# Kernel optimization log

Measured on AMD Instinct MI355X. Metric: run time of the kernel, lower is better.

Reference implementation:

```python
import jax, jax.numpy as jnp
import numpy as np

NEG_SLOPE = 0.2  # PyG GATConv default leaky_relu slope


def gat_conv(x, src, dst, W, att_src, att_dst, bias, num_nodes):
    """PyG-style GATConv with concat=False (mean over heads).
    x: [N, Fin], src/dst: [E] (self-loops already appended),
    W: [Fin, H*C], att_src/att_dst: [H, C], bias: [C].
    """
    H, C = att_src.shape
    h = (x @ W).reshape(num_nodes, H, C)               # [N, H, C]
    a_s = jnp.sum(h * att_src[None], axis=-1)          # [N, H]
    a_d = jnp.sum(h * att_dst[None], axis=-1)          # [N, H]
    e = jax.nn.leaky_relu(a_s[src] + a_d[dst], NEG_SLOPE)  # [E, H]
    # softmax over incoming edges per destination node
    e_max = jax.ops.segment_max(e, dst, num_segments=num_nodes)  # [N, H]
    e_exp = jnp.exp(e - e_max[dst])
    denom = jax.ops.segment_sum(e_exp, dst, num_segments=num_nodes)
    alpha = e_exp / (denom[dst] + 1e-16)               # [E, H]
    msg = h[src] * alpha[:, :, None]                   # [E, H, C]
    out = jax.ops.segment_sum(msg, dst, num_segments=num_nodes)  # [N, H, C]
    return out.mean(axis=1) + bias                     # concat=False -> head mean


def setup_inputs() -> dict:
    N, E = 100000, 1600000
    Fin, Hid, Fout, Hds = 128, 64, 32, 2
    key = jax.random.key(0)
    ks = jax.random.split(key, 12)
    glorot = lambda k, shape, fan: (jax.random.normal(k, shape, jnp.float32) / np.sqrt(fan))
    return {
        "x": jax.random.normal(ks[0], (N, Fin), jnp.float32),
        "edge_index": jax.random.randint(ks[1], (2, E), 0, N, jnp.int64 if jax.config.read("jax_enable_x64") else jnp.int32),
        "W1": glorot(ks[2], (Fin, Hds * Hid), Fin),
        "att_src1": glorot(ks[3], (Hds, Hid), Hid),
        "att_dst1": glorot(ks[4], (Hds, Hid), Hid),
        "b1": jnp.zeros((Hid,), jnp.float32),
        "W2": glorot(ks[5], (Hid, Hds * Fout), Hid),
        "att_src2": glorot(ks[6], (Hds, Fout), Fout),
        "att_dst2": glorot(ks[7], (Hds, Fout), Fout),
        "b2": jnp.zeros((Fout,), jnp.float32),
    }


def reference(x, edge_index, W1, att_src1, att_dst1, b1, W2, att_src2, att_dst2, b2):
    N = x.shape[0]
    # PyG GATConv default: add self-loops
    loops = jnp.arange(N, dtype=edge_index.dtype)
    src = jnp.concatenate([edge_index[0], loops])
    dst = jnp.concatenate([edge_index[1], loops])
    # dropout(p=0.6) is identity in eval mode
    h = gat_conv(x, src, dst, W1, att_src1, att_dst1, b1, N)
    h = jax.nn.elu(h)
    out = gat_conv(h, src, dst, W2, att_src2, att_dst2, b2, N)
    return out
```

## Files before the change

### kernel.cpp

```cpp
#include <hip/hip_runtime.h>
#include <hip/hip_bf16.h>
#include <hip/hip_fp16.h>
#include <math.h>


#define BINBITS 9
#define NBUCK 256
#define CHUNK 4096
#define SPANCAP 12288


__global__ void init_kernel(int* __restrict__ bcnt) {
    bcnt[threadIdx.x] = 0;
}

__global__ void bucket_hist_kernel(const int* __restrict__ dst, int* __restrict__ bcnt, int E) {
    __shared__ int h[NBUCK];
    int t = threadIdx.x;
    h[t] = 0;
    __syncthreads();
    for (int i = blockIdx.x * blockDim.x + t; i < E; i += gridDim.x * blockDim.x)
        atomicAdd(&h[dst[i] >> BINBITS], 1);
    __syncthreads();
    if (h[t]) atomicAdd(&bcnt[t], h[t]);
}

__global__ void bucket_scan_kernel(const int* __restrict__ bcnt, int* __restrict__ bbase,
                                   int* __restrict__ bfill) {
    __shared__ int sd[NBUCK];
    int t = threadIdx.x;
    int v = bcnt[t];
    sd[t] = v;
    __syncthreads();
    for (int o = 1; o < NBUCK; o <<= 1) {
        int x = (t >= o) ? sd[t - o] : 0;
        __syncthreads();
        sd[t] += x;
        __syncthreads();
    }
    int exc = sd[t] - v;
    bbase[t] = exc;
    bfill[t] = exc;
    if (t == NBUCK - 1) bbase[NBUCK] = sd[t];
}

__launch_bounds__(256)
__global__ void binA_kernel(const int* __restrict__ esrc, const int* __restrict__ edst,
                            int* __restrict__ bfill, unsigned* __restrict__ binned, int E) {
    __shared__ unsigned stage[CHUNK];
    __shared__ int hcnt[NBUCK], hexc[NBUCK], gb[NBUCK], hfill[NBUCK];
    const int tid = threadIdx.x;
    const int c0 = blockIdx.x * CHUNK;
    const int n = min(CHUNK, E - c0);

    hcnt[tid] = 0;
    hfill[tid] = 0;
    __syncthreads();
    for (int i = tid; i < n; i += 256) atomicAdd(&hcnt[edst[c0 + i] >> BINBITS], 1);
    __syncthreads();
    int myc = hcnt[tid];
    hexc[tid] = myc;
    __syncthreads();
    for (int o = 1; o < NBUCK; o <<= 1) {
        int x = (tid >= o) ? hexc[tid - o] : 0;
        __syncthreads();
        hexc[tid] += x;
        __syncthreads();
    }
    hexc[tid] -= myc;
    gb[tid] = myc ? atomicAdd(&bfill[tid], myc) : 0;
    __syncthreads();

    for (int i = tid; i < n; i += 256) {
        int d = edst[c0 + i], s = esrc[c0 + i];
        int b = d >> BINBITS;
        int p = hexc[b] + atomicAdd(&hfill[b], 1);
        stage[p] = ((unsigned)(d & ((1 << BINBITS) - 1)) << 17) | (unsigned)s;
    }
    __syncthreads();

    const int wid = tid >> 6, lane = tid & 63;
    for (int b = wid * 64; b < wid * 64 + 64; ++b) {
        int cnt = hcnt[b], sb = hexc[b], g = gb[b];
        for (int l = lane; l < cnt; l += 64) binned[g + l] = stage[sb + l];
    }
}

__launch_bounds__(256)
__global__ void binB_kernel(const unsigned* __restrict__ binned, const int* __restrict__ bbase,
                            int* __restrict__ rowptr, int* __restrict__ csr, int N) {
    __shared__ int cnt[512];
    __shared__ int chunk[256];
    __shared__ int excl[513];
    __shared__ int stag[SPANCAP];
    const int tid = threadIdx.x;
    const int b = blockIdx.x;
    const int node0 = b << BINBITS;
    if (node0 >= N) return;
    const int nn = min(512, N - node0);

    cnt[tid] = (tid < nn) ? 1 : 0;
    cnt[tid + 256] = (tid + 256 < nn) ? 1 : 0;
    __syncthreads();
    const int e0 = bbase[b], e1 = bbase[b + 1];
    for (int i = e0 + tid; i < e1; i += 256)
        atomicAdd(&cnt[binned[i] >> 17], 1);
    __syncthreads();

    int c0v = cnt[2 * tid], c1v = cnt[2 * tid + 1];
    chunk[tid] = c0v + c1v;
    __syncthreads();
    int v = chunk[tid];
    for (int o = 1; o < 256; o <<= 1) {
        int x = (tid >= o) ? chunk[tid - o] : 0;
        __syncthreads();
        chunk[tid] += x;
        __syncthreads();
    }
    int cpre = chunk[tid] - v;
    excl[2 * tid] = cpre;
    excl[2 * tid + 1] = cpre + c0v;
    if (tid == 255) excl[512] = cpre + c0v + c1v;
    __syncthreads();

    const int rbase = e0 + node0;
    for (int i = tid; i < nn; i += 256) rowptr[node0 + i] = rbase + excl[i];
    if (node0 + nn >= N && tid == 0) rowptr[N] = rbase + excl[512];

    cnt[tid] = 0;
    cnt[tid + 256] = 0;
    __syncthreads();
    const int span = excl[512];

    if (span <= SPANCAP) {
        for (int i = e0 + tid; i < e1; i += 256) {
            unsigned e = binned[i];
            int dloc = e >> 17, src = e & 0x1FFFF;
            int p = excl[dloc] + atomicAdd(&cnt[dloc], 1);
            stag[p] = src;
        }
        for (int i = tid; i < nn; i += 256) {
            int p = excl[i] + atomicAdd(&cnt[i], 1);
            stag[p] = node0 + i;
        }
        __syncthreads();
        for (int i = tid; i < span; i += 256) csr[rbase + i] = stag[i];
    } else {
        for (int i = e0 + tid; i < e1; i += 256) {
            unsigned e = binned[i];
            int dloc = e >> 17, src = e & 0x1FFFF;
            csr[rbase + excl[dloc] + atomicAdd(&cnt[dloc], 1)] = src;
        }
        for (int i = tid; i < nn; i += 256)
            csr[rbase + excl[i] + atomicAdd(&cnt[i], 1)] = node0 + i;
    }
}


template <int FIN, int FOUT, int TM, int KC>
__launch_bounds__(256)
__global__ void gemm_attn_kernel(const float* __restrict__ X, const float* __restrict__ Wg,
                                 const float* __restrict__ atts, const float* __restrict__ attd,
                                 __half* __restrict__ Hh, float* __restrict__ a_s,
                                 float* __restrict__ a_d, int N) {
    constexpr int COLG = FOUT / 8;
    constexpr int ROWG = 256 / COLG;
    constexpr int BM = ROWG * TM;
    constexpr int C = FOUT / 2;
    constexpr int PR = BM + 4;
    __shared__ float sW[KC * FOUT];
    __shared__ float sX[KC * PR];

    const int tid = threadIdx.x;
    const int tc = tid % COLG;
    const int tr = tid / COLG;
    const int row0 = blockIdx.x * BM;

    float accA[TM][4], accB[TM][4];
#pragma unroll
    for (int i = 0; i < TM; ++i)
#pragma unroll
        for (int j = 0; j < 4; ++j) { accA[i][j] = 0.f; accB[i][j] = 0.f; }

    for (int kc = 0; kc < FIN; kc += KC) {
        __syncthreads();
        for (int idx = tid; idx < KC * FOUT / 4; idx += 256) {
            int k = idx / (FOUT / 4), cq = idx % (FOUT / 4);
            *(float4*)&sW[k * FOUT + cq * 4] =
                *(const float4*)&Wg[(size_t)(kc + k) * FOUT + cq * 4];
        }
        for (int idx = tid; idx < BM * KC / 4; idx += 256) {
            int r = idx / (KC / 4), kq = idx % (KC / 4);
            int gr = row0 + r;
            float4 v = make_float4(0.f, 0.f, 0.f, 0.f);
            if (gr < N) v = *(const float4*)&X[(size_t)gr * FIN + kc + kq * 4];
            sX[(kq * 4 + 0) * PR + r] = v.x;
            sX[(kq * 4 + 1) * PR + r] = v.y;
            sX[(kq * 4 + 2) * PR + r] = v.z;
            sX[(kq * 4 + 3) * PR + r] = v.w;
        }
        __syncthreads();
#pragma unroll 4
        for (int k = 0; k < KC; ++k) {
            float xv[TM];
#pragma unroll
            for (int q = 0; q < TM / 4; ++q)
                *(float4*)&xv[q * 4] = *(const float4*)&sX[k * PR + tr * TM + q * 4];
            float wa[4], wb[4];
            *(float4*)wa = *(const float4*)&sW[k * FOUT + tc * 4];
            *(float4*)wb = *(const float4*)&sW[k * FOUT + C + tc * 4];
#pragma unroll
            for (int i = 0; i < TM; ++i) {
#pragma unroll
                for (int j = 0; j < 4; ++j) {
                    accA[i][j] = fmaf(xv[i], wa[j], accA[i][j]);
                    accB[i][j] = fmaf(xv[i], wb[j], accB[i][j]);
                }
            }
        }
    }

    float aSA[4], aSB[4], aDA[4], aDB[4];
#pragma unroll
    for (int j = 0; j < 4; ++j) {
        aSA[j] = atts[tc * 4 + j];
        aSB[j] = atts[C + tc * 4 + j];
        aDA[j] = attd[tc * 4 + j];
        aDB[j] = attd[C + tc * 4 + j];
    }

#pragma unroll
    for (int i = 0; i < TM; ++i) {
        int gr = row0 + tr * TM + i;
        if (gr < N) {
            union { int2 i2; __half2 h2[2]; } u;
            u.h2[0] = __halves2half2(__float2half(accA[i][0]), __float2half(accA[i][1]));
            u.h2[1] = __halves2half2(__float2half(accA[i][2]), __float2half(accA[i][3]));
            *reinterpret_cast<int2*>(&Hh[(size_t)gr * FOUT + tc * 4]) = u.i2;
            u.h2[0] = __halves2half2(__float2half(accB[i][0]), __float2half(accB[i][1]));
            u.h2[1] = __halves2half2(__float2half(accB[i][2]), __float2half(accB[i][3]));
            *reinterpret_cast<int2*>(&Hh[(size_t)gr * FOUT + C + tc * 4]) = u.i2;
        }
        float ps0 = 0.f, ps1 = 0.f, pd0 = 0.f, pd1 = 0.f;
#pragma unroll
        for (int j = 0; j < 4; ++j) {
            ps0 = fmaf(accA[i][j], aSA[j], ps0);
            ps1 = fmaf(accB[i][j], aSB[j], ps1);
            pd0 = fmaf(accA[i][j], aDA[j], pd0);
            pd1 = fmaf(accB[i][j], aDB[j], pd1);
        }
#pragma unroll
        for (int o = 1; o < COLG; o <<= 1) {
            ps0 += __shfl_xor(ps0, o);
            ps1 += __shfl_xor(ps1, o);
            pd0 += __shfl_xor(pd0, o);
            pd1 += __shfl_xor(pd1, o);
        }
        if (tc == 0 && gr < N) {
            *(float2*)&a_s[gr * 2] = make_float2(ps0, ps1);
            *(float2*)&a_d[gr * 2] = make_float2(pd0, pd1);
        }
    }
}


__device__ __forceinline__ float lrelu02(float x) { return x > 0.f ? x : 0.2f * x; }

__launch_bounds__(256)
__global__ void edge_w_kernel(const float* __restrict__ a_s, const float* __restrict__ a_d,
                              const int* __restrict__ rowptr, const int* __restrict__ csr,
                              float2* __restrict__ w, int N) {
    const int wid = threadIdx.x >> 6, lane = threadIdx.x & 63;
    int n = blockIdx.x * 4 + wid;
    if (n >= N) return;
    int start = rowptr[n], end = rowptr[n + 1];
    float2 adn = ((const float2*)a_d)[n];
    float d0 = 0.f, d1 = 0.f;
    for (int j = start + lane; j < end; j += 64) {
        int s = csr[j];
        float2 asv = ((const float2*)a_s)[s];
        float e0 = __expf(lrelu02(asv.x + adn.x));
        float e1 = __expf(lrelu02(asv.y + adn.y));
        d0 += e0;
        d1 += e1;
        w[j] = make_float2(e0, e1);
    }
#pragma unroll
    for (int o = 32; o > 0; o >>= 1) {
        d0 += __shfl_xor(d0, o);
        d1 += __shfl_xor(d1, o);
    }
    float i0 = 0.5f / d0, i1 = 0.5f / d1;
    for (int j = start + lane; j < end; j += 64) {
        float2 f = w[j];
        w[j] = make_float2(f.x * i0, f.y * i1);
    }
}


template <int C, bool ELU>
__launch_bounds__(256)
__global__ void aggregate_kernel(const __half* __restrict__ Hh, const float2* __restrict__ w,
                                 const int* __restrict__ rowptr, const int* __restrict__ csr,
                                 const float* __restrict__ bias, float* __restrict__ out, int N) {
    __shared__ float2 swH[4][64][2];
    const int wid = threadIdx.x >> 6;
    const int lane = threadIdx.x & 63;
    const int hp = lane >> 5;
    const int sub = lane & 31;
    const int head = sub >> 4;
    const int chq = sub & 15;
    int n = blockIdx.x * 4 + wid;
    if (n >= N) return;
    int start = rowptr[n], end = rowptr[n + 1];

    float acc0 = 0.f, acc1 = 0.f, acc2 = 0.f, acc3 = 0.f;

    for (int cs = start; cs < end; cs += 64) {
        int j = cs + lane;
        float2 wv = make_float2(0.f, 0.f);
        int s = 0;
        if (j < end) {
            s = csr[j];
            wv = w[j];
        }
        float fs = __int_as_float(s);
        swH[wid][lane][0] = make_float2(wv.x, fs);
        swH[wid][lane][1] = make_float2(wv.y, fs);
        int cnt = min(64, end - cs);
        int npair = (cnt + 1) >> 1;
        for (int p0 = 0; p0 < npair; p0 += 4) {
            float2 e[4];
#pragma unroll
            for (int u = 0; u < 4; ++u)
                e[u] = swH[wid][2 * (p0 + u) + hp][head];
            if (C == 64) {
                ushort4 hv[4];
#pragma unroll
                for (int u = 0; u < 4; ++u)
                    hv[u] = ((const ushort4*)Hh)[(size_t)__float_as_int(e[u].y) * 32 + sub];
#pragma unroll
                for (int u = 0; u < 4; ++u) {
                    const __half* hx = (const __half*)&hv[u];
                    acc0 = fmaf(e[u].x, __half2float(hx[0]), acc0);
                    acc1 = fmaf(e[u].x, __half2float(hx[1]), acc1);
                    acc2 = fmaf(e[u].x, __half2float(hx[2]), acc2);
                    acc3 = fmaf(e[u].x, __half2float(hx[3]), acc3);
                }
            } else {
                __half2 hv[4];
#pragma unroll
                for (int u = 0; u < 4; ++u)
                    hv[u] = ((const __half2*)Hh)[(size_t)__float_as_int(e[u].y) * 32 + sub];
#pragma unroll
                for (int u = 0; u < 4; ++u) {
                    float2 v = __half22float2(hv[u]);
                    acc0 = fmaf(e[u].x, v.x, acc0);
                    acc1 = fmaf(e[u].x, v.y, acc1);
                }
            }
        }
    }

    acc0 += __shfl_xor(acc0, 32);
    acc1 += __shfl_xor(acc1, 32);
    if (C == 64) {
        acc2 += __shfl_xor(acc2, 32);
        acc3 += __shfl_xor(acc3, 32);
    }
    acc0 += __shfl_xor(acc0, 16);
    acc1 += __shfl_xor(acc1, 16);
    if (C == 64) {
        acc2 += __shfl_xor(acc2, 16);
        acc3 += __shfl_xor(acc3, 16);
    }

    if (lane < 16) {
        if (C == 64) {
            float4 bv = *(const float4*)(bias + chq * 4);
            float o0 = acc0 + bv.x;
            float o1 = acc1 + bv.y;
            float o2 = acc2 + bv.z;
            float o3 = acc3 + bv.w;
            if (ELU) {
                o0 = o0 > 0.f ? o0 : expm1f(o0);
                o1 = o1 > 0.f ? o1 : expm1f(o1);
                o2 = o2 > 0.f ? o2 : expm1f(o2);
                o3 = o3 > 0.f ? o3 : expm1f(o3);
            }
            *(float4*)(out + (size_t)n * 64 + chq * 4) = make_float4(o0, o1, o2, o3);
        } else {
            float2 bv = *(const float2*)(bias + chq * 2);
            float o0 = acc0 + bv.x;
            float o1 = acc1 + bv.y;
            if (ELU) {
                o0 = o0 > 0.f ? o0 : expm1f(o0);
                o1 = o1 > 0.f ? o1 : expm1f(o1);
            }
            *(float2*)(out + (size_t)n * 32 + chq * 2) = make_float2(o0, o1);
        }
    }
}


extern "C" void kernel_launch(void* const* d_in, const int* in_sizes, int n_in,
                              void* d_out, int out_size, void* d_ws, size_t ws_size,
                              hipStream_t stream) {
    const float* x    = (const float*)d_in[0];
    const int*   eidx = (const int*)d_in[1];
    const float* W1   = (const float*)d_in[2];
    const float* as1w = (const float*)d_in[3];
    const float* ad1w = (const float*)d_in[4];
    const float* b1   = (const float*)d_in[5];
    const float* W2   = (const float*)d_in[6];
    const float* as2w = (const float*)d_in[7];
    const float* ad2w = (const float*)d_in[8];
    const float* b2   = (const float*)d_in[9];
    float* out = (float*)d_out;

    const int N = in_sizes[0] / 128;
    const int E = in_sizes[1] / 2;
    const int NBK = (N + (1 << BINBITS) - 1) >> BINBITS;

    char* base = (char*)d_ws;
    size_t off = 0;
    auto alloc = [&](size_t bytes) {
        size_t cur = off;
        off += (bytes + 255) & ~(size_t)255;
        return (void*)(base + cur);
    };

    int* rowptr   = (int*)alloc((size_t)(N + 1) * 4);
    int* csr      = (int*)alloc((size_t)(E + N) * 4);
    int* bcnt     = (int*)alloc((size_t)NBUCK * 4);
    int* bbase    = (int*)alloc((size_t)(NBUCK + 1) * 4);
    int* bfill    = (int*)alloc((size_t)NBUCK * 4);
    unsigned* binned = (unsigned*)alloc((size_t)E * 4);
    __half* h1    = (__half*)alloc((size_t)N * 128 * 2);
    float* x2     = (float*)alloc((size_t)N * 64 * 4);
    float* a_s    = (float*)alloc((size_t)N * 2 * 4);
    float* a_d    = (float*)alloc((size_t)N * 2 * 4);
    float2* wEdge = (float2*)alloc((size_t)(E + N) * 8);

    const int* esrc = eidx;
    const int* edst = eidx + E;

    init_kernel<<<1, NBUCK, 0, stream>>>(bcnt);
    bucket_hist_kernel<<<256, 256, 0, stream>>>(edst, bcnt, E);
    bucket_scan_kernel<<<1, NBUCK, 0, stream>>>(bcnt, bbase, bfill);
    binA_kernel<<<(E + CHUNK - 1) / CHUNK, 256, 0, stream>>>(esrc, edst, bfill, binned, E);
    binB_kernel<<<NBK, 256, 0, stream>>>(binned, bbase, rowptr, csr, N);

    gemm_attn_kernel<128, 128, 8, 32>
        <<<(N + 127) / 128, 256, 0, stream>>>(x, W1, as1w, ad1w, h1, a_s, a_d, N);
    edge_w_kernel<<<(N + 3) / 4, 256, 0, stream>>>(a_s, a_d, rowptr, csr, wEdge, N);
    aggregate_kernel<64, true><<<(N + 3) / 4, 256, 0, stream>>>(h1, wEdge, rowptr, csr, b1, x2, N);

    gemm_attn_kernel<64, 64, 4, 32>
        <<<(N + 127) / 128, 256, 0, stream>>>(x2, W2, as2w, ad2w, h1, a_s, a_d, N);
    edge_w_kernel<<<(N + 3) / 4, 256, 0, stream>>>(a_s, a_d, rowptr, csr, wEdge, N);
    aggregate_kernel<32, false><<<(N + 3) / 4, 256, 0, stream>>>(h1, wEdge, rowptr, csr, b2, out, N);
}
```

Before: 396.9 us.

## Use fp16 MFMA for node projection GEMMs and store hidden features in fp16

Replaces the scalar fp32 FMA GEMM with a matrix-core kernel using 16x16x32 fp16 MFMA, with weights pre-transposed and converted to fp16 by a small kernel. The first layer's aggregation now writes its ELU output in fp16, which the second GEMM reads directly, halving that intermediate's traffic. Attention logits are computed from the MFMA accumulators, and the H tile is staged through shared memory for coalesced stores. Inputs are rounded to fp16 before the multiply, which lowers precision. The whole A tile sits in shared memory (about 64 KB for layer 1), which may limit occupancy.

```diff
diff --git a/kernel.cpp b/kernel.cpp
--- a/kernel.cpp
+++ b/kernel.cpp
@@ -8,6 +8,9 @@
 #define NBUCK 256
 #define CHUNK 4096
 #define SPANCAP 12288
+
+typedef _Float16 half8 __attribute__((ext_vector_type(8)));
+typedef float f32x4 __attribute__((ext_vector_type(4)));
 
 
 __global__ void init_kernel(int* __restrict__ bcnt) {
@@ -157,109 +160,139 @@
 }
 
 
-template <int FIN, int FOUT, int TM, int KC>
+__global__ void wcvt_kernel(const float* __restrict__ W, _Float16* __restrict__ Wt,
+                            int K, int Fout) {
+    int i = blockIdx.x * 256 + threadIdx.x;
+    if (i < K * Fout) {
+        int n = i / K, k = i % K;
+        Wt[i] = (_Float16)W[k * Fout + n];
+    }
+}
+
+
+template <int FIN, int FOUT, typename XT>
 __launch_bounds__(256)
-__global__ void gemm_attn_kernel(const float* __restrict__ X, const float* __restrict__ Wg,
-                                 const float* __restrict__ atts, const float* __restrict__ attd,
-                                 __half* __restrict__ Hh, float* __restrict__ a_s,
-                                 float* __restrict__ a_d, int N) {
-    constexpr int COLG = FOUT / 8;
-    constexpr int ROWG = 256 / COLG;
-    constexpr int BM = ROWG * TM;
+__global__ void gemm_attn_mfma(const XT* __restrict__ X, const _Float16* __restrict__ Wt,
+                               const float* __restrict__ atts, const float* __restrict__ attd,
+                               __half* __restrict__ Hh, float* __restrict__ a_s,
+                               float* __restrict__ a_d, int N) {
+    constexpr int BM = 128;
     constexpr int C = FOUT / 2;
-    constexpr int PR = BM + 4;
-    __shared__ float sW[KC * FOUT];
-    __shared__ float sX[KC * PR];
+    constexpr int NT = FOUT / 16;
+    constexpr int KS = FIN / 32;
+    constexpr int HT = C / 16;
+    __shared__ _Float16 sA[BM * FIN];
+    __shared__ _Float16 sB[FOUT * FIN];
 
     const int tid = threadIdx.x;
-    const int tc = tid % COLG;
-    const int tr = tid / COLG;
+    const int wv = tid >> 6, ln = tid & 63;
+    const int lm = ln & 15, quad = ln >> 4;
     const int row0 = blockIdx.x * BM;
 
-    float accA[TM][4], accB[TM][4];
-#pragma unroll
-    for (int i = 0; i < TM; ++i)
-#pragma unroll
-        for (int j = 0; j < 4; ++j) { accA[i][j] = 0.f; accB[i][j] = 0.f; }
-
-    for (int kc = 0; kc < FIN; kc += KC) {
-        __syncthreads();
-        for (int idx = tid; idx < KC * FOUT / 4; idx += 256) {
-            int k = idx / (FOUT / 4), cq = idx % (FOUT / 4);
-            *(float4*)&sW[k * FOUT + cq * 4] =
-                *(const float4*)&Wg[(size_t)(kc + k) * FOUT + cq * 4];
-        }
-        for (int idx = tid; idx < BM * KC / 4; idx += 256) {
-            int r = idx / (KC / 4), kq = idx % (KC / 4);
+    if (sizeof(XT) == 4) {
+        for (int idx = tid; idx < BM * FIN / 4; idx += 256) {
+            int r = idx / (FIN / 4), c4 = idx % (FIN / 4);
             int gr = row0 + r;
             float4 v = make_float4(0.f, 0.f, 0.f, 0.f);
-            if (gr < N) v = *(const float4*)&X[(size_t)gr * FIN + kc + kq * 4];
-            sX[(kq * 4 + 0) * PR + r] = v.x;
-            sX[(kq * 4 + 1) * PR + r] = v.y;
-            sX[(kq * 4 + 2) * PR + r] = v.z;
-            sX[(kq * 4 + 3) * PR + r] = v.w;
-        }
-        __syncthreads();
-#pragma unroll 4
-        for (int k = 0; k < KC; ++k) {
-            float xv[TM];
-#pragma unroll
-            for (int q = 0; q < TM / 4; ++q)
-                *(float4*)&xv[q * 4] = *(const float4*)&sX[k * PR + tr * TM + q * 4];
-            float wa[4], wb[4];
-            *(float4*)wa = *(const float4*)&sW[k * FOUT + tc * 4];
-            *(float4*)wb = *(const float4*)&sW[k * FOUT + C + tc * 4];
-#pragma unroll
-            for (int i = 0; i < TM; ++i) {
-#pragma unroll
-                for (int j = 0; j < 4; ++j) {
-                    accA[i][j] = fmaf(xv[i], wa[j], accA[i][j]);
-                    accB[i][j] = fmaf(xv[i], wb[j], accB[i][j]);
+            if (gr < N) v = *(const float4*)&((const float*)X)[(size_t)gr * FIN + c4 * 4];
+            _Float16 h4[4] = {(_Float16)v.x, (_Float16)v.y, (_Float16)v.z, (_Float16)v.w};
+            *(float2*)&sA[r * FIN + c4 * 4] = *(float2*)h4;
+        }
+    } else {
+        for (int idx = tid; idx < BM * FIN / 8; idx += 256) {
+            int r = idx / (FIN / 8), c8 = idx % (FIN / 8);
+            int gr = row0 + r;
+            int4 v = make_int4(0, 0, 0, 0);
+            if (gr < N) v = *(const int4*)&((const __half*)X)[(size_t)gr * FIN + c8 * 8];
+            *(int4*)&sA[r * FIN + c8 * 8] = v;
+        }
+    }
+    for (int idx = tid; idx < FOUT * FIN / 8; idx += 256)
+        *(int4*)&sB[idx * 8] = *(const int4*)&Wt[idx * 8];
+    __syncthreads();
+
+    f32x4 acc[2][NT];
+#pragma unroll
+    for (int mt = 0; mt < 2; ++mt)
+#pragma unroll
+        for (int nt = 0; nt < NT; ++nt) acc[mt][nt] = f32x4{0.f, 0.f, 0.f, 0.f};
+
+    const int r0 = wv * 32 + lm;
+#pragma unroll
+    for (int ks = 0; ks < KS; ++ks) {
+        int k0 = ks * 32 + quad * 8;
+        half8 a0 = *(const half8*)&sA[r0 * FIN + k0];
+        half8 a1 = *(const half8*)&sA[(r0 + 16) * FIN + k0];
+#pragma unroll
+        for (int nt = 0; nt < NT; ++nt) {
+            half8 b = *(const half8*)&sB[(nt * 16 + lm) * FIN + k0];
+            acc[0][nt] = __builtin_amdgcn_mfma_f32_16x16x32_f16(a0, b, acc[0][nt], 0, 0, 0);
+            acc[1][nt] = __builtin_amdgcn_mfma_f32_16x16x32_f16(a1, b, acc[1][nt], 0, 0, 0);
+        }
+    }
+
+    float psum[2][4][2], pdum[2][4][2];
+#pragma unroll
+    for (int mt = 0; mt < 2; ++mt)
+#pragma unroll
+        for (int r = 0; r < 4; ++r) {
+            psum[mt][r][0] = psum[mt][r][1] = 0.f;
+            pdum[mt][r][0] = pdum[mt][r][1] = 0.f;
+        }
+#pragma unroll
+    for (int nt = 0; nt < NT; ++nt) {
+        float av = atts[nt * 16 + lm];
+        float dv = attd[nt * 16 + lm];
+        int hh = nt / HT;
+#pragma unroll
+        for (int mt = 0; mt < 2; ++mt)
+#pragma unroll
+            for (int r = 0; r < 4; ++r) {
+                psum[mt][r][hh] = fmaf(acc[mt][nt][r], av, psum[mt][r][hh]);
+                pdum[mt][r][hh] = fmaf(acc[mt][nt][r], dv, pdum[mt][r][hh]);
+            }
+    }
+#pragma unroll
+    for (int o = 1; o < 16; o <<= 1) {
+#pragma unroll
+        for (int mt = 0; mt < 2; ++mt)
+#pragma unroll
+            for (int r = 0; r < 4; ++r) {
+                psum[mt][r][0] += __shfl_xor(psum[mt][r][0], o);
+                psum[mt][r][1] += __shfl_xor(psum[mt][r][1], o);
+                pdum[mt][r][0] += __shfl_xor(pdum[mt][r][0], o);
+                pdum[mt][r][1] += __shfl_xor(pdum[mt][r][1], o);
+            }
+    }
+    if (lm == 0) {
+#pragma unroll
+        for (int mt = 0; mt < 2; ++mt)
+#pragma unroll
+            for (int r = 0; r < 4; ++r) {
+                int gr = row0 + wv * 32 + mt * 16 + quad * 4 + r;
+                if (gr < N) {
+                    *(float2*)&a_s[gr * 2] = make_float2(psum[mt][r][0], psum[mt][r][1]);
+                    *(float2*)&a_d[gr * 2] = make_float2(pdum[mt][r][0], pdum[mt][r][1]);
                 }
             }
-        }
-    }
-
-    float aSA[4], aSB[4], aDA[4], aDB[4];
-#pragma unroll
-    for (int j = 0; j < 4; ++j) {
-        aSA[j] = atts[tc * 4 + j];
-        aSB[j] = atts[C + tc * 4 + j];
-        aDA[j] = attd[tc * 4 + j];
-        aDB[j] = attd[C + tc * 4 + j];
-    }
-
-#pragma unroll
-    for (int i = 0; i < TM; ++i) {
-        int gr = row0 + tr * TM + i;
-        if (gr < N) {
-            union { int2 i2; __half2 h2[2]; } u;
-            u.h2[0] = __halves2half2(__float2half(accA[i][0]), __float2half(accA[i][1]));
-            u.h2[1] = __halves2half2(__float2half(accA[i][2]), __float2half(accA[i][3]));
-            *reinterpret_cast<int2*>(&Hh[(size_t)gr * FOUT + tc * 4]) = u.i2;
-            u.h2[0] = __halves2half2(__float2half(accB[i][0]), __float2half(accB[i][1]));
-            u.h2[1] = __halves2half2(__float2half(accB[i][2]), __float2half(accB[i][3]));
-            *reinterpret_cast<int2*>(&Hh[(size_t)gr * FOUT + C + tc * 4]) = u.i2;
-        }
-        float ps0 = 0.f, ps1 = 0.f, pd0 = 0.f, pd1 = 0.f;
-#pragma unroll
-        for (int j = 0; j < 4; ++j) {
-            ps0 = fmaf(accA[i][j], aSA[j], ps0);
-            ps1 = fmaf(accB[i][j], aSB[j], ps1);
-            pd0 = fmaf(accA[i][j], aDA[j], pd0);
-            pd1 = fmaf(accB[i][j], aDB[j], pd1);
-        }
-#pragma unroll
-        for (int o = 1; o < COLG; o <<= 1) {
-            ps0 += __shfl_xor(ps0, o);
-            ps1 += __shfl_xor(ps1, o);
-            pd0 += __shfl_xor(pd0, o);
-            pd1 += __shfl_xor(pd1, o);
-        }
-        if (tc == 0 && gr < N) {
-            *(float2*)&a_s[gr * 2] = make_float2(ps0, ps1);
-            *(float2*)&a_d[gr * 2] = make_float2(pd0, pd1);
-        }
+    }
+
+    __syncthreads();
+    _Float16* sH = sA;
+#pragma unroll
+    for (int mt = 0; mt < 2; ++mt)
+#pragma unroll
+        for (int nt = 0; nt < NT; ++nt)
+#pragma unroll
+            for (int r = 0; r < 4; ++r)
+                sH[(wv * 32 + mt * 16 + quad * 4 + r) * FOUT + nt * 16 + lm] =
+                    (_Float16)acc[mt][nt][r];
+    __syncthreads();
+    for (int idx = tid; idx < BM * FOUT / 8; idx += 256) {
+        int r = idx / (FOUT / 8), c8 = idx % (FOUT / 8);
+        int gr = row0 + r;
+        if (gr < N)
+            *(int4*)&Hh[(size_t)gr * FOUT + c8 * 8] = *(const int4*)&sH[r * FOUT + c8 * 8];
     }
 }
 
@@ -298,11 +331,11 @@
 }
 
 
-template <int C, bool ELU>
+template <int C, bool ELU, typename OT>
 __launch_bounds__(256)
 __global__ void aggregate_kernel(const __half* __restrict__ Hh, const float2* __restrict__ w,
                                  const int* __restrict__ rowptr, const int* __restrict__ csr,
-                                 const float* __restrict__ bias, float* __restrict__ out, int N) {
+                                 const float* __restrict__ bias, OT* __restrict__ out, int N) {
     __shared__ float2 swH[4][64][2];
     const int wid = threadIdx.x >> 6;
     const int lane = threadIdx.x & 63;
@@ -388,7 +421,15 @@
                 o2 = o2 > 0.f ? o2 : expm1f(o2);
                 o3 = o3 > 0.f ? o3 : expm1f(o3);
             }
-            *(float4*)(out + (size_t)n * 64 + chq * 4) = make_float4(o0, o1, o2, o3);
+            if (sizeof(OT) == 2) {
+                __half2 p0 = __floats2half2_rn(o0, o1);
+                __half2 p1 = __floats2half2_rn(o2, o3);
+                ((__half2*)out)[(size_t)n * 32 + chq * 2] = p0;
+                ((__half2*)out)[(size_t)n * 32 + chq * 2 + 1] = p1;
+            } else {
+                *(float4*)((float*)out + (size_t)n * 64 + chq * 4) =
+                    make_float4(o0, o1, o2, o3);
+            }
         } else {
             float2 bv = *(const float2*)(bias + chq * 2);
             float o0 = acc0 + bv.x;
@@ -397,7 +438,7 @@
                 o0 = o0 > 0.f ? o0 : expm1f(o0);
                 o1 = o1 > 0.f ? o1 : expm1f(o1);
             }
-            *(float2*)(out + (size_t)n * 32 + chq * 2) = make_float2(o0, o1);
+            *(float2*)((float*)out + (size_t)n * 32 + chq * 2) = make_float2(o0, o1);
         }
     }
 }
@@ -437,10 +478,12 @@
     int* bfill    = (int*)alloc((size_t)NBUCK * 4);
     unsigned* binned = (unsigned*)alloc((size_t)E * 4);
     __half* h1    = (__half*)alloc((size_t)N * 128 * 2);
-    float* x2     = (float*)alloc((size_t)N * 64 * 4);
+    __half* x2h   = (__half*)alloc((size_t)N * 64 * 2);
     float* a_s    = (float*)alloc((size_t)N * 2 * 4);
     float* a_d    = (float*)alloc((size_t)N * 2 * 4);
     float2* wEdge = (float2*)alloc((size_t)(E + N) * 8);
+    _Float16* Wt1 = (_Float16*)alloc((size_t)128 * 128 * 2);
+    _Float16* Wt2 = (_Float16*)alloc((size_t)64 * 64 * 2);
 
     const int* esrc = eidx;
     const int* edst = eidx + E;
@@ -451,13 +494,18 @@
     binA_kernel<<<(E + CHUNK - 1) / CHUNK, 256, 0, stream>>>(esrc, edst, bfill, binned, E);
     binB_kernel<<<NBK, 256, 0, stream>>>(binned, bbase, rowptr, csr, N);
 
-    gemm_attn_kernel<128, 128, 8, 32>
-        <<<(N + 127) / 128, 256, 0, stream>>>(x, W1, as1w, ad1w, h1, a_s, a_d, N);
+    wcvt_kernel<<<(128 * 128 + 255) / 256, 256, 0, stream>>>(W1, Wt1, 128, 128);
+    wcvt_kernel<<<(64 * 64 + 255) / 256, 256, 0, stream>>>(W2, Wt2, 64, 64);
+
+    gemm_attn_mfma<128, 128, float>
+        <<<(N + 127) / 128, 256, 0, stream>>>(x, Wt1, as1w, ad1w, h1, a_s, a_d, N);
     edge_w_kernel<<<(N + 3) / 4, 256, 0, stream>>>(a_s, a_d, rowptr, csr, wEdge, N);
-    aggregate_kernel<64, true><<<(N + 3) / 4, 256, 0, stream>>>(h1, wEdge, rowptr, csr, b1, x2, N);
-
-    gemm_attn_kernel<64, 64, 4, 32>
-        <<<(N + 127) / 128, 256, 0, stream>>>(x2, W2, as2w, ad2w, h1, a_s, a_d, N);
+    aggregate_kernel<64, true, __half>
+        <<<(N + 3) / 4, 256, 0, stream>>>(h1, wEdge, rowptr, csr, b1, x2h, N);
+
+    gemm_attn_mfma<64, 64, __half>
+        <<<(N + 127) / 128, 256, 0, stream>>>(x2h, Wt2, as2w, ad2w, h1, a_s, a_d, N);
     edge_w_kernel<<<(N + 3) / 4, 256, 0, stream>>>(a_s, a_d, rowptr, csr, wEdge, N);
-    aggregate_kernel<32, false><<<(N + 3) / 4, 256, 0, stream>>>(h1, wEdge, rowptr, csr, b2, out, N);
-}
+    aggregate_kernel<32, false, float>
+        <<<(N + 3) / 4, 256, 0, stream>>>(h1, wEdge, rowptr, csr, b2, out, N);
+}
```

After: 374.6 us. 5.6% less time.
